# Optimization experiments

Hardware: AMD Instinct MI355X
Metric: run time of the kernel (lower is better)

The kernel has to match this reference:

```python
import jax, jax.numpy as jnp
import numpy as np

N = 16383        # complete binary tree, 14 levels
D_NODE = 512
D_SSM = 512
D_STATE = 16
MAX_DEPTH = 14   # number of BFS levels (depth 0..13)
LN_EPS = 1e-5


def setup_inputs() -> dict:
    key = jax.random.key(0)
    ks = jax.random.split(key, 8)
    # tree structure: parent[i] = (i-1)//2, root has parent -1; BFS order == index order
    parent = np.concatenate([np.array([-1]), (np.arange(1, N) - 1) // 2]).astype(np.int64)
    depth = np.floor(np.log2(np.arange(N) + 1)).astype(np.int32)
    s = jax.random.normal(ks[0], (N, D_NODE), jnp.float32)
    w = jax.random.uniform(ks[1], (N,), jnp.float32, minval=0.01, maxval=1.0)
    # parameters (xavier-ish scales)
    W_in = jax.random.normal(ks[2], (D_SSM, D_NODE + 1), jnp.float32) * (1.0 / np.sqrt(D_NODE + 1))
    b_in = jnp.zeros((D_SSM,), jnp.float32)
    W_delta = jax.random.normal(ks[3], (D_SSM, D_SSM), jnp.float32) * (1.0 / np.sqrt(D_SSM))
    # dt-style bias init: softplus(b) ~ dt in [1e-3, 1e-1]
    dt = jnp.exp(jax.random.uniform(ks[4], (D_SSM,), jnp.float32) * (np.log(0.1) - np.log(0.001)) + np.log(0.001))
    b_delta = dt + jnp.log(-jnp.expm1(-dt))
    W_w = jax.random.normal(ks[5], (D_SSM, 1), jnp.float32)
    b_w = jnp.zeros((D_SSM,), jnp.float32)
    A_log = jnp.log(jnp.broadcast_to(jnp.arange(1.0, D_STATE + 1.0, dtype=jnp.float32)[None, :], (D_SSM, D_STATE)))
    D = jnp.ones((D_SSM,), jnp.float32)
    W_B = jax.random.normal(ks[6], (D_STATE, D_SSM), jnp.float32) * (1.0 / np.sqrt(D_SSM))
    b_B = jnp.zeros((D_STATE,), jnp.float32)
    W_C = jax.random.normal(ks[7], (D_STATE, D_SSM), jnp.float32) * (1.0 / np.sqrt(D_SSM))
    b_C = jnp.zeros((D_STATE,), jnp.float32)
    gamma = jnp.ones((D_SSM,), jnp.float32)
    beta = jnp.zeros((D_SSM,), jnp.float32)
    return {"s": s, "w": w, "parent": jnp.asarray(parent), "depth": jnp.asarray(depth),
            "W_in": W_in, "b_in": b_in, "W_delta": W_delta, "b_delta": b_delta,
            "W_w": W_w, "b_w": b_w, "A_log": A_log, "D": D,
            "W_B": W_B, "b_B": b_B, "W_C": W_C, "b_C": b_C,
            "gamma": gamma, "beta": beta}


def reference(s, w, parent, depth, W_in, b_in, W_delta, b_delta, W_w, b_w,
              A_log, D, W_B, b_B, W_C, b_C, gamma, beta):
    n = s.shape[0]
    log_w = jnp.log(w + 1e-6)[:, None]                       # [N, 1]
    feat = jnp.concatenate([s, log_w], axis=1)               # [N, d_node+1]
    x = feat @ W_in.T + b_in                                 # [N, d_ssm]
    delta = jax.nn.softplus(x @ W_delta.T + b_delta) * jax.nn.sigmoid(log_w @ W_w.T + b_w)  # [N, d_ssm]
    A = -jnp.exp(A_log)                                      # [d_ssm, d_state]
    B = x @ W_B.T + b_B                                      # [N, d_state]
    C = x @ W_C.T + b_C                                      # [N, d_state]
    A_bar = jnp.exp(delta[:, :, None] * A[None])             # [N, d_ssm, d_state]
    Bx = (delta * x)[:, :, None] * B[:, None, :]             # [N, d_ssm, d_state]
    # level-parallel tree scan: all nodes at BFS depth l updated together
    par = jnp.maximum(parent, 0)
    has_par = (parent >= 0)[:, None, None]
    H = jnp.zeros((n, A_bar.shape[1], A_bar.shape[2]), x.dtype)
    for lvl in range(MAX_DEPTH):
        h_par = jnp.where(has_par, jnp.take(H, par, axis=0), 0.0)
        H = jnp.where((depth == lvl)[:, None, None], A_bar * h_par + Bx, H)
    Y = jnp.einsum('nds,ns->nd', H, C) + D * x               # [N, d_ssm]
    mu = jnp.mean(Y, axis=-1, keepdims=True)
    var = jnp.var(Y, axis=-1, keepdims=True)
    return (Y - mu) / jnp.sqrt(var + LN_EPS) * gamma + beta
```

## Files before the change

kernel.cpp:

```cpp
#include <hip/hip_runtime.h>
#include <hip/hip_bf16.h>
#include <math.h>

#define D_SSM 512
#define D_STATE 16
#define CKPT_BASE 511
#define N_CKPT 512
#define MPAD 16384

typedef __attribute__((ext_vector_type(8))) short short8;
typedef __attribute__((ext_vector_type(4))) float floatx4;

__device__ __forceinline__ unsigned short f2bf(float f) {
    unsigned int u = __float_as_uint(f);
    unsigned int r = (u + 0x7fffu + ((u >> 16) & 1u)) >> 16;
    return (unsigned short)r;
}
__device__ __forceinline__ float bf2f(unsigned short u) {
    return __uint_as_float(((unsigned int)u) << 16);
}
__device__ __forceinline__ void g2lds16(const void* g, void* l) {
    __builtin_amdgcn_global_load_lds(
        (const __attribute__((address_space(1))) void*)g,
        (__attribute__((address_space(3))) void*)l, 16, 0, 0);
}

__device__ __forceinline__ void pw_powers(float r, float* p) {
    float r2 = r * r, r4 = r2 * r2, r8 = r4 * r4;
    p[0] = r;          p[1] = r2;         p[2] = r2 * r;     p[3] = r4;
    p[4] = r4 * r;     p[5] = r4 * r2;    p[6] = r4 * p[2];  p[7] = r8;
    p[8] = r8 * r;     p[9] = r8 * r2;    p[10] = r8 * p[2]; p[11] = r8 * r4;
    p[12] = r8 * p[4]; p[13] = r8 * p[5]; p[14] = r8 * p[6]; p[15] = r8 * r8;
}

__global__ __launch_bounds__(256) void prep_kernel(
    const float* __restrict__ s, const float* __restrict__ w,
    const float* __restrict__ W_in, const float* __restrict__ W_delta,
    const float* __restrict__ W_B, const float* __restrict__ W_C,
    const float* __restrict__ A_log,
    unsigned short* __restrict__ s_bf, float* __restrict__ lw,
    unsigned short* __restrict__ Win_bf, unsigned short* __restrict__ Wd_bf,
    float* __restrict__ As_tab, int* __restrict__ fast_tab,
    int Nn)
{
    const int b = blockIdx.x, t = threadIdx.x;
    if (b < 2048) {
        #pragma unroll
        for (int rr = 0; rr < 8; rr++) {
            int row = b * 8 + rr;
            unsigned int pack = 0;
            if (row < Nn) {
                float2 sv = *(const float2*)(s + (size_t)row * 512 + t * 2);
                pack = (unsigned int)f2bf(sv.x) | ((unsigned int)f2bf(sv.y) << 16);
            }
            *(unsigned int*)(s_bf + (size_t)row * 512 + t * 2) = pack;
            if (t == 0) lw[row] = (row < Nn) ? logf(w[row] + 1e-6f) : 0.f;
        }
    } else if (b < 2048 + 512) {
        int c = b - 2048;
        float a0 = W_in[(size_t)c * 513 + t * 2];
        float a1 = W_in[(size_t)c * 513 + t * 2 + 1];
        *(unsigned int*)(Win_bf + (size_t)c * 512 + t * 2) =
            (unsigned int)f2bf(a0) | ((unsigned int)f2bf(a1) << 16);
    } else if (b < 2048 + 1024) {
        int c = b - 2048 - 512;
        float2 wv = *(const float2*)(W_delta + (size_t)c * 512 + t * 2);
        *(unsigned int*)(Wd_bf + (size_t)c * 512 + t * 2) =
            (unsigned int)f2bf(wv.x) | ((unsigned int)f2bf(wv.y) << 16);
    } else if (b < 2048 + 1024 + 128) {
        int c = b - 2048 - 1024;
        float2 wv; wv.x = 0.f; wv.y = 0.f;
        if (c < 16)      wv = *(const float2*)(W_B + (size_t)c * 512 + t * 2);
        else if (c < 32) wv = *(const float2*)(W_C + (size_t)(c - 16) * 512 + t * 2);
        *(unsigned int*)(Wd_bf + (size_t)(512 + c) * 512 + t * 2) =
            (unsigned int)f2bf(wv.x) | ((unsigned int)f2bf(wv.y) << 16);
    } else {
        int ch = (b - (2048 + 1024 + 128)) * 256 + t;
        float As0 = -__expf(A_log[ch * 16]);
        bool ok = true;
        #pragma unroll
        for (int q = 1; q < 16; q++) {
            float As = -__expf(A_log[ch * 16 + q]);
            ok = ok && (fabsf(As - (float)(q + 1) * As0) <= 1e-4f * (float)(q + 1));
        }
        As_tab[ch] = As0;
        fast_tab[ch] = ok ? 1 : 0;
    }
}

__global__ __launch_bounds__(256) void gemm_mfma(
    const unsigned short* __restrict__ Abf,
    const unsigned short* __restrict__ Wbf,
    float* __restrict__ outf,
    unsigned short* __restrict__ outbf,
    const float* __restrict__ bias,
    const float* __restrict__ lw,
    const float* __restrict__ wcol, int wcol_stride,
    const float* __restrict__ bw,
    const float* __restrict__ b_B, const float* __restrict__ b_C,
    float* __restrict__ Bm, float* __restrict__ Cm,
    int mode)
{
    __shared__ __align__(16) short As[2][128 * 32];
    __shared__ __align__(16) short Bs[2][128 * 32];
    const int tid = threadIdx.x;
    const int wave = tid >> 6, lane = tid & 63;

    const int nwg  = gridDim.x * gridDim.y;
    const int orig = blockIdx.y * gridDim.x + blockIdx.x;
    const int wsw  = (orig & 7) * (nwg >> 3) + (orig >> 3);
    const int bx   = wsw % gridDim.x;
    const int by   = wsw / gridDim.x;
    const int row0 = by * 128;
    const int col0 = bx * 128;

    const int wr = (wave >> 1) * 64;
    const int wc = (wave & 1) * 64;

    floatx4 acc[4][4] = {};

    const int srow = lane >> 2;
    const int sg   = (lane & 3) ^ ((srow >> 1) & 3);
    const int scol = sg * 8;

    const unsigned short* Ag = Abf + (size_t)(row0 + wave * 16 + srow) * 512 + scol;
    const unsigned short* Wg = Wbf + (size_t)(col0 + wave * 16 + srow) * 512 + scol;
    char* Al = (char*)&As[0][0] + wave * 1024;
    char* Bl = (char*)&Bs[0][0] + wave * 1024;

    #define STAGE(buf, k0)                                              \
        do {                                                            \
            g2lds16(Ag + (k0),            Al + (buf) * 8192);           \
            g2lds16(Ag + 64 * 512 + (k0), Al + (buf) * 8192 + 4096);    \
            g2lds16(Wg + (k0),            Bl + (buf) * 8192);           \
            g2lds16(Wg + 64 * 512 + (k0), Bl + (buf) * 8192 + 4096);    \
        } while (0)

    STAGE(0, 0);
    __syncthreads();

    for (int it = 0; it < 16; ++it) {
        const int cur = it & 1;
        if (it < 15) STAGE(cur ^ 1, (it + 1) * 32);

        short8 af[4], bfr[4];
        #pragma unroll
        for (int i = 0; i < 4; i++) {
            int m = wr + i * 16 + (lane & 15);
            int gm = (lane >> 4) ^ ((m >> 1) & 3);
            af[i] = *(const short8*)&As[cur][m * 32 + gm * 8];
        }
        #pragma unroll
        for (int j = 0; j < 4; j++) {
            int n = wc + j * 16 + (lane & 15);
            int gn = (lane >> 4) ^ ((n >> 1) & 3);
            bfr[j] = *(const short8*)&Bs[cur][n * 32 + gn * 8];
        }
        #pragma unroll
        for (int i = 0; i < 4; i++)
            #pragma unroll
            for (int j = 0; j < 4; j++)
                acc[i][j] = __builtin_amdgcn_mfma_f32_16x16x32_bf16(af[i], bfr[j], acc[i][j], 0, 0, 0);
        __syncthreads();
    }
    #undef STAGE

    if (col0 >= 512) {
        #pragma unroll
        for (int i = 0; i < 4; i++) {
            #pragma unroll
            for (int reg = 0; reg < 4; reg++) {
                int r = row0 + wr + i * 16 + (lane >> 4) * 4 + reg;
                #pragma unroll
                for (int j = 0; j < 4; j++) {
                    int c2 = wc + j * 16 + (lane & 15);
                    float z = acc[i][j][reg];
                    if (c2 < 16)      Bm[(size_t)r * 16 + c2]        = z + b_B[c2];
                    else if (c2 < 32) Cm[(size_t)r * 16 + (c2 - 16)] = z + b_C[c2 - 16];
                }
            }
        }
        return;
    }

    #pragma unroll
    for (int i = 0; i < 4; i++) {
        #pragma unroll
        for (int reg = 0; reg < 4; reg++) {
            int r = row0 + wr + i * 16 + (lane >> 4) * 4 + reg;
            float lwr = lw[r];
            #pragma unroll
            for (int j = 0; j < 4; j++) {
                int c = col0 + wc + j * 16 + (lane & 15);
                float z = acc[i][j][reg] + bias[c];
                if (mode == 0) {
                    float o = z + lwr * wcol[(size_t)c * wcol_stride];
                    outbf[(size_t)r * 512 + c] = f2bf(o);
                } else {
                    float sp = (z > 15.f) ? z : __logf(1.f + __expf(z));
                    float sg2 = __builtin_amdgcn_rcpf(1.f + __expf(-(lwr * wcol[c] + bw[c])));
                    outf[(size_t)r * 512 + c] = sp * sg2;
                }
            }
        }
    }
}

__global__ __launch_bounds__(512) void scan_fused(
    const unsigned short* __restrict__ x_bf, const float* __restrict__ delta,
    const float* __restrict__ Bm, const float* __restrict__ Cm,
    const float* __restrict__ A_log, const float* __restrict__ Dv,
    const float* __restrict__ gamma, const float* __restrict__ beta,
    const float* __restrict__ As_tab, const int* __restrict__ fast_tab,
    float* __restrict__ out)
{
    __shared__ __align__(16) float SMEM[16 * 512 + 31 * 32 + 10 * 16];
    __shared__ int nid[16];
    const int bid = blockIdx.x;
    const int d = threadIdx.x;

    const float As0 = As_tab[d];
    const bool fast = fast_tab[d] != 0;
    const float dvd = Dv[d];

    if (bid < 2 * N_CKPT) {
        const int p  = bid & 511;
        const int c0 = bid >> 9;
        const int a9 = CKPT_BASE + p;
        float* const Yb   = SMEM;
        float* const BCs  = SMEM + 8192;
        float* const Banc = SMEM + 8192 + 992;

        for (int idx = d; idx < 31 * 32; idx += 512) {
            int i = idx >> 5, c = idx & 31;
            int v = i + 1;
            int j = 31 - __builtin_clz((unsigned)v);
            int node = ((a9 + 1) << j) - 1 + (v - (1 << j));
            BCs[i * 32 + c] = (c < 16) ? Bm[(size_t)node * 16 + c]
                                       : Cm[(size_t)node * 16 + (c - 16)];
        }
        if (d < 160) {
            int k = d >> 4, ss = d & 15;
            int a = a9;
            for (int q = 0; q < k; q++) a = (a - 1) >> 1;
            Banc[k * 16 + ss] = Bm[(size_t)a * 16 + ss];
        }

        const int n10 = 2 * a9 + 1 + c0;
        float cd, nd1, nd2, nd3;
        unsigned short cx, nx1, nx2, nx3;
        cd  = delta[(size_t)n10 * 512 + d];
        cx  = x_bf[(size_t)n10 * 512 + d];
        nd1 = delta[(size_t)(2 * n10 + 1) * 512 + d];
        nx1 = x_bf[(size_t)(2 * n10 + 1) * 512 + d];
        nd2 = delta[(size_t)(4 * n10 + 3) * 512 + d];
        nx2 = x_bf[(size_t)(4 * n10 + 3) * 512 + d];

        int aB = (a9 - 1) >> 1;
        float adA = delta[(size_t)a9 * 512 + d];
        float adB = delta[(size_t)aB * 512 + d];
        unsigned short axA = x_bf[(size_t)a9 * 512 + d];
        unsigned short axB = x_bf[(size_t)aB * 512 + d];
        int anext = (aB - 1) >> 1;

        __syncthreads();

        float H9v[16];
        #pragma unroll
        for (int ss = 0; ss < 16; ss++) H9v[ss] = 0.f;
        float xv0 = 0.f;
        {
            float cum = 0.f;
            #pragma unroll
            for (int k = 0; k < 10; k++) {
                float da = adA;
                float xvk = bf2f(axA);
                if (k == 0) xv0 = xvk;
                adA = adB; axA = axB;
                if (k < 8) {
                    adB = delta[(size_t)anext * 512 + d];
                    axB = x_bf[(size_t)anext * 512 + d];
                    anext = (anext - 1) >> 1;
                }
                float bx = da * xvk;
                if (fast) {
                    float r = __expf(As0 * cum);
                    float pw[16]; pw_powers(r, pw);
                    const floatx4* B4 = (const floatx4*)&Banc[k * 16];
                    #pragma unroll
                    for (int q = 0; q < 4; q++) {
                        floatx4 b = B4[q];
                        #pragma unroll
                        for (int u = 0; u < 4; u++) {
                            int ss = q * 4 + u;
                            H9v[ss] = fmaf(bx * pw[ss], b[u], H9v[ss]);
                        }
                    }
                } else {
                    #pragma unroll
                    for (int ss = 0; ss < 16; ss++) {
                        float As = -__expf(A_log[d * 16 + ss]);
                        H9v[ss] = fmaf(bx * __expf(As * cum), Banc[k * 16 + ss], H9v[ss]);
                    }
                }
                cum += da;
            }
        }

        auto stepf = [&](int n, int bfs, float dlt, unsigned short xraw,
                         const float* Hp, float* Hc, int slot) {
            float xv = bf2f(xraw);
            float bx = dlt * xv;
            const floatx4* B4 = (const floatx4*)&BCs[bfs * 32];
            const floatx4* C4 = (const floatx4*)&BCs[bfs * 32 + 16];
            float y0 = 0.f, y1 = 0.f;
            if (fast) {
                float r = __expf(As0 * dlt);
                float pw[16]; pw_powers(r, pw);
                #pragma unroll
                for (int q = 0; q < 4; q++) {
                    floatx4 b = B4[q], c = C4[q];
                    #pragma unroll
                    for (int u = 0; u < 4; u++) {
                        int ss = q * 4 + u;
                        Hc[ss] = fmaf(pw[ss], Hp[ss], bx * b[u]);
                        if (ss & 1) y1 = fmaf(c[u], Hc[ss], y1);
                        else        y0 = fmaf(c[u], Hc[ss], y0);
                    }
                }
            } else {
                #pragma unroll
                for (int ss = 0; ss < 16; ss++) {
                    float Ab = __expf(dlt * (-__expf(A_log[d * 16 + ss])));
                    Hc[ss] = fmaf(Ab, Hp[ss], bx * BCs[bfs * 32 + ss]);
                    float cc = BCs[bfs * 32 + 16 + ss];
                    if (ss & 1) y1 = fmaf(cc, Hc[ss], y1);
                    else        y0 = fmaf(cc, Hc[ss], y0);
                }
            }
            Yb[slot * 512 + d] = fmaf(dvd, xv, y0 + y1);
            if (d == 0) nid[slot] = n;
        };
        auto leaff = [&](int n, int bfs, float dlt, unsigned short xraw,
                         const float* Hp, int slot) {
            float xv = bf2f(xraw);
            float bx = dlt * xv;
            const floatx4* B4 = (const floatx4*)&BCs[bfs * 32];
            const floatx4* C4 = (const floatx4*)&BCs[bfs * 32 + 16];
            float y0 = 0.f, y1 = 0.f;
            if (fast) {
                float r = __expf(As0 * dlt);
                float pw[16]; pw_powers(r, pw);
                #pragma unroll
                for (int q = 0; q < 4; q++) {
                    floatx4 b = B4[q], c = C4[q];
                    #pragma unroll
                    for (int u = 0; u < 4; u++) {
                        int ss = q * 4 + u;
                        float h = fmaf(pw[ss], Hp[ss], bx * b[u]);
                        if (ss & 1) y1 = fmaf(c[u], h, y1);
                        else        y0 = fmaf(c[u], h, y0);
                    }
                }
            } else {
                #pragma unroll
                for (int ss = 0; ss < 16; ss++) {
                    float Ab = __expf(dlt * (-__expf(A_log[d * 16 + ss])));
                    float h = fmaf(Ab, Hp[ss], bx * BCs[bfs * 32 + ss]);
                    float cc = BCs[bfs * 32 + 16 + ss];
                    if (ss & 1) y1 = fmaf(cc, h, y1);
                    else        y0 = fmaf(cc, h, y0);
                }
            }
            Yb[slot * 512 + d] = fmaf(dvd, xv, y0 + y1);
            if (d == 0) nid[slot] = n;
        };

        int slot = 0;
        if (c0 == 0) {
            const floatx4* C4 = (const floatx4*)&BCs[16];
            float y0 = 0.f, y1 = 0.f;
            #pragma unroll
            for (int q = 0; q < 4; q++) {
                floatx4 c = C4[q];
                #pragma unroll
                for (int u = 0; u < 4; u++) {
                    int ss = q * 4 + u;
                    if (ss & 1) y1 = fmaf(c[u], H9v[ss], y1);
                    else        y0 = fmaf(c[u], H9v[ss], y0);
                }
            }
            Yb[d] = fmaf(dvd, xv0, y0 + y1);
            if (d == 0) nid[0] = a9;
            slot = 1;
        }

        float H10[16], H11[16], H12[16];
        #define PREF(NODE) do { nd3 = delta[(size_t)(NODE) * 512 + d]; \
                                nx3 = x_bf[(size_t)(NODE) * 512 + d]; } while (0)
        #define ROT() do { cd = nd1; cx = nx1; nd1 = nd2; nx1 = nx2; \
                           nd2 = nd3; nx2 = nx3; } while (0)
        PREF(8 * n10 + 7);   stepf(n10,          1 + c0,    cd, cx, H9v, H10, slot++); ROT();
        PREF(8 * n10 + 8);   stepf(2 * n10 + 1,  3 + 2*c0,  cd, cx, H10, H11, slot++); ROT();
        PREF(4 * n10 + 4);   stepf(4 * n10 + 3,  7 + 4*c0,  cd, cx, H11, H12, slot++); ROT();
        PREF(8 * n10 + 9);   leaff(8 * n10 + 7,  15 + 8*c0, cd, cx, H12, slot++); ROT();
        PREF(8 * n10 + 10);  leaff(8 * n10 + 8,  16 + 8*c0, cd, cx, H12, slot++); ROT();
        PREF(2 * n10 + 2);   stepf(4 * n10 + 4,  8 + 4*c0,  cd, cx, H11, H12, slot++); ROT();
        PREF(4 * n10 + 5);   leaff(8 * n10 + 9,  17 + 8*c0, cd, cx, H12, slot++); ROT();
        PREF(8 * n10 + 11);  leaff(8 * n10 + 10, 18 + 8*c0, cd, cx, H12, slot++); ROT();
        PREF(8 * n10 + 12);  stepf(2 * n10 + 2,  4 + 2*c0,  cd, cx, H10, H11, slot++); ROT();
        PREF(4 * n10 + 6);   stepf(4 * n10 + 5,  9 + 4*c0,  cd, cx, H11, H12, slot++); ROT();
        PREF(8 * n10 + 13);  leaff(8 * n10 + 11, 19 + 8*c0, cd, cx, H12, slot++); ROT();
        PREF(8 * n10 + 14);  leaff(8 * n10 + 12, 20 + 8*c0, cd, cx, H12, slot++); ROT();
                             stepf(4 * n10 + 6,  10 + 4*c0, cd, cx, H11, H12, slot++); ROT();
                             leaff(8 * n10 + 13, 21 + 8*c0, cd, cx, H12, slot++); ROT();
                             leaff(8 * n10 + 14, 22 + 8*c0, cd, cx, H12, slot++);
        #undef PREF
        #undef ROT
        __syncthreads();

        const int cnt = (c0 == 0) ? 16 : 15;
        const int w = d >> 6, lane = d & 63;
        for (int i = w; i < cnt; i += 8) {
            int n = nid[i];
            float v[8]; float s1 = 0.f, s2 = 0.f;
            #pragma unroll
            for (int k = 0; k < 8; k++) {
                v[k] = Yb[i * 512 + lane + 64 * k];
                s1 += v[k]; s2 += v[k] * v[k];
            }
            #pragma unroll
            for (int off = 32; off > 0; off >>= 1) {
                s1 += __shfl_xor(s1, off);
                s2 += __shfl_xor(s2, off);
            }
            float mu = s1 * (1.f / 512.f);
            float inv = rsqrtf(s2 * (1.f / 512.f) - mu * mu + 1e-5f);
            #pragma unroll
            for (int k = 0; k < 8; k++) {
                int ch = lane + 64 * k;
                out[(size_t)n * 512 + ch] = (v[k] - mu) * inv * gamma[ch] + beta[ch];
            }
        }
    } else {
        const int n = bid - 2 * N_CKPT;
        float* const Banc9 = SMEM;
        float* const Cn    = SMEM + 144;
        float* const red   = SMEM + 160;

        if (d < 144) {
            int k = d >> 4, ss = d & 15;
            int a = n;
            for (int q = 0; q < 9; q++) if (q < k) a = (a < 0) ? -1 : ((a - 1) >> 1);
            Banc9[k * 16 + ss] = (a >= 0) ? Bm[(size_t)a * 16 + ss] : 0.f;
        }
        if (d >= 240 && d < 256) Cn[d - 240] = Cm[(size_t)n * 16 + (d - 240)];

        float adl[9]; unsigned short axr[9];
        {
            int a = n;
            #pragma unroll
            for (int k = 0; k < 9; k++) {
                bool v = a >= 0;
                adl[k] = v ? delta[(size_t)a * 512 + d] : 0.f;
                axr[k] = v ? x_bf[(size_t)a * 512 + d] : (unsigned short)0;
                a = v ? ((a - 1) >> 1) : -1;
            }
        }
        __syncthreads();

        float acc[16];
        #pragma unroll
        for (int ss = 0; ss < 16; ss++) acc[ss] = 0.f;

        float cum = 0.f;
        #pragma unroll
        for (int k = 0; k < 9; k++) {
            float da = adl[k];
            float bx = da * bf2f(axr[k]);
            if (fast) {
                float r = __expf(As0 * cum);
                float pw[16]; pw_powers(r, pw);
                const floatx4* B4 = (const floatx4*)&Banc9[k * 16];
                #pragma unroll
                for (int q = 0; q < 4; q++) {
                    floatx4 b = B4[q];
                    #pragma unroll
                    for (int u = 0; u < 4; u++) {
                        int ss = q * 4 + u;
                        acc[ss] = fmaf(bx * pw[ss], b[u], acc[ss]);
                    }
                }
            } else {
                #pragma unroll
                for (int ss = 0; ss < 16; ss++) {
                    float As = -__expf(A_log[d * 16 + ss]);
                    acc[ss] = fmaf(bx * __expf(As * cum), Banc9[k * 16 + ss], acc[ss]);
                }
            }
            cum += da;
        }

        float xv = bf2f(axr[0]);
        float y0 = 0.f, y1 = 0.f;
        const floatx4* C4 = (const floatx4*)&Cn[0];
        #pragma unroll
        for (int q = 0; q < 4; q++) {
            floatx4 c = C4[q];
            #pragma unroll
            for (int u = 0; u < 4; u++) {
                int ss = q * 4 + u;
                if (ss & 1) y1 = fmaf(c[u], acc[ss], y1);
                else        y0 = fmaf(c[u], acc[ss], y0);
            }
        }
        float y = fmaf(dvd, xv, y0 + y1);

        float s1 = y, s2 = y * y;
        #pragma unroll
        for (int off = 32; off > 0; off >>= 1) {
            s1 += __shfl_xor(s1, off);
            s2 += __shfl_xor(s2, off);
        }
        int wid = d >> 6, lane = d & 63;
        if (lane == 0) { red[wid] = s1; red[wid + 8] = s2; }
        __syncthreads();
        float S1 = 0.f, S2 = 0.f;
        #pragma unroll
        for (int k = 0; k < 8; k++) { S1 += red[k]; S2 += red[k + 8]; }
        float mu = S1 * (1.f / 512.f);
        float var = S2 * (1.f / 512.f) - mu * mu;
        float inv = rsqrtf(var + 1e-5f);
        out[(size_t)n * 512 + d] = (y - mu) * inv * gamma[d] + beta[d];
    }
}

extern "C" void kernel_launch(void* const* d_in, const int* in_sizes, int n_in,
                              void* d_out, int out_size, void* d_ws, size_t ws_size,
                              hipStream_t stream) {
    const float* s_in   = (const float*)d_in[0];
    const float* w      = (const float*)d_in[1];
    const float* W_in    = (const float*)d_in[4];
    const float* b_in    = (const float*)d_in[5];
    const float* W_delta = (const float*)d_in[6];
    const float* b_delta = (const float*)d_in[7];
    const float* W_w     = (const float*)d_in[8];
    const float* b_w     = (const float*)d_in[9];
    const float* A_log   = (const float*)d_in[10];
    const float* Dv      = (const float*)d_in[11];
    const float* W_B     = (const float*)d_in[12];
    const float* b_B     = (const float*)d_in[13];
    const float* W_C     = (const float*)d_in[14];
    const float* b_C     = (const float*)d_in[15];
    const float* gamma   = (const float*)d_in[16];
    const float* beta    = (const float*)d_in[17];
    float* out = (float*)d_out;

    const int Nn = in_sizes[1];

    float* ws    = (float*)d_ws;
    float* lw    = ws;
    float* delta = lw + MPAD;
    float* Bm    = delta + (size_t)MPAD * 512;
    float* Cm    = Bm + (size_t)MPAD * 16;
    unsigned short* s_bf  = (unsigned short*)(Cm + (size_t)MPAD * 16);
    unsigned short* x_bf  = s_bf + (size_t)MPAD * 512;
    unsigned short* Win_bf = x_bf + (size_t)MPAD * 512;
    unsigned short* Wd_bf  = Win_bf + 512 * 512;
    float* As_tab  = (float*)(Wd_bf + 640 * 512);
    int*   fast_tab = (int*)(As_tab + 512);

    prep_kernel<<<2048 + 1024 + 128 + 2, 256, 0, stream>>>(
        s_in, w, W_in, W_delta, W_B, W_C, A_log,
        s_bf, lw, Win_bf, Wd_bf, As_tab, fast_tab, Nn);

    dim3 g1(4, 128);
    gemm_mfma<<<g1, 256, 0, stream>>>(s_bf, Win_bf, nullptr, x_bf,
                                      b_in, lw, W_in + 512, 513, nullptr,
                                      nullptr, nullptr, nullptr, nullptr, 0);
    dim3 g2(5, 128);
    gemm_mfma<<<g2, 256, 0, stream>>>(x_bf, Wd_bf, delta, nullptr,
                                      b_delta, lw, W_w, 1, b_w,
                                      b_B, b_C, Bm, Cm, 1);

    scan_fused<<<2 * N_CKPT + CKPT_BASE, 512, 0, stream>>>(
        x_bf, delta, Bm, Cm, A_log, Dv, gamma, beta, As_tab, fast_tab, out);
}
```

Baseline: 215.6 us.

## Merge both checkpoint subtrees into one block to share ancestor scan work

Each checkpoint block now processes both child subtrees of its level-9 node instead of launching two blocks, one per child. Each child previously recomputed the ancestor chain state (H9) and the shared loads. The merged block computes it once, flushes layer norm output between the two subtrees, and halves the number of checkpoint blocks. The cost is less parallelism (fewer, longer blocks) and an extra barrier and flush phase inside each block.

```diff
diff --git a/kernel.cpp b/kernel.cpp
--- a/kernel.cpp
+++ b/kernel.cpp
@@ -223,10 +223,10 @@
     const bool fast = fast_tab[d] != 0;
     const float dvd = Dv[d];
 
-    if (bid < 2 * N_CKPT) {
-        const int p  = bid & 511;
-        const int c0 = bid >> 9;
-        const int a9 = CKPT_BASE + p;
+    if (bid < N_CKPT) {
+        const int a9 = CKPT_BASE + bid;
+        const int t0 = 2 * a9 + 1;
+        const int t1 = 2 * a9 + 2;
         float* const Yb   = SMEM;
         float* const BCs  = SMEM + 8192;
         float* const Banc = SMEM + 8192 + 992;
@@ -246,15 +246,12 @@
             Banc[k * 16 + ss] = Bm[(size_t)a * 16 + ss];
         }
 
-        const int n10 = 2 * a9 + 1 + c0;
-        float cd, nd1, nd2, nd3;
-        unsigned short cx, nx1, nx2, nx3;
-        cd  = delta[(size_t)n10 * 512 + d];
-        cx  = x_bf[(size_t)n10 * 512 + d];
-        nd1 = delta[(size_t)(2 * n10 + 1) * 512 + d];
-        nx1 = x_bf[(size_t)(2 * n10 + 1) * 512 + d];
-        nd2 = delta[(size_t)(4 * n10 + 3) * 512 + d];
-        nx2 = x_bf[(size_t)(4 * n10 + 3) * 512 + d];
+        float cd, nd1, nd2;
+        unsigned short cx, nx1, nx2;
+        cd  = delta[(size_t)t0 * 512 + d];
+        cx  = x_bf[(size_t)t0 * 512 + d];
+        nd1 = delta[(size_t)(2 * t0 + 1) * 512 + d];
+        nx1 = x_bf[(size_t)(2 * t0 + 1) * 512 + d];
 
         int aB = (a9 - 1) >> 1;
         float adA = delta[(size_t)a9 * 512 + d];
@@ -375,9 +372,32 @@
             Yb[slot * 512 + d] = fmaf(dvd, xv, y0 + y1);
             if (d == 0) nid[slot] = n;
         };
-
-        int slot = 0;
-        if (c0 == 0) {
+        auto flush = [&](int cnt) {
+            const int w = d >> 6, lane = d & 63;
+            for (int i = w; i < cnt; i += 8) {
+                int n = nid[i];
+                float v[8]; float s1 = 0.f, s2 = 0.f;
+                #pragma unroll
+                for (int k = 0; k < 8; k++) {
+                    v[k] = Yb[i * 512 + lane + 64 * k];
+                    s1 += v[k]; s2 += v[k] * v[k];
+                }
+                #pragma unroll
+                for (int off = 32; off > 0; off >>= 1) {
+                    s1 += __shfl_xor(s1, off);
+                    s2 += __shfl_xor(s2, off);
+                }
+                float mu = s1 * (1.f / 512.f);
+                float inv = rsqrtf(s2 * (1.f / 512.f) - mu * mu + 1e-5f);
+                #pragma unroll
+                for (int k = 0; k < 8; k++) {
+                    int ch = lane + 64 * k;
+                    out[(size_t)n * 512 + ch] = (v[k] - mu) * inv * gamma[ch] + beta[ch];
+                }
+            }
+        };
+
+        {
             const floatx4* C4 = (const floatx4*)&BCs[16];
             float y0 = 0.f, y1 = 0.f;
             #pragma unroll
@@ -392,58 +412,51 @@
             }
             Yb[d] = fmaf(dvd, xv0, y0 + y1);
             if (d == 0) nid[0] = a9;
-            slot = 1;
         }
 
         float H10[16], H11[16], H12[16];
-        #define PREF(NODE) do { nd3 = delta[(size_t)(NODE) * 512 + d]; \
-                                nx3 = x_bf[(size_t)(NODE) * 512 + d]; } while (0)
-        #define ROT() do { cd = nd1; cx = nx1; nd1 = nd2; nx1 = nx2; \
-                           nd2 = nd3; nx2 = nx3; } while (0)
-        PREF(8 * n10 + 7);   stepf(n10,          1 + c0,    cd, cx, H9v, H10, slot++); ROT();
-        PREF(8 * n10 + 8);   stepf(2 * n10 + 1,  3 + 2*c0,  cd, cx, H10, H11, slot++); ROT();
-        PREF(4 * n10 + 4);   stepf(4 * n10 + 3,  7 + 4*c0,  cd, cx, H11, H12, slot++); ROT();
-        PREF(8 * n10 + 9);   leaff(8 * n10 + 7,  15 + 8*c0, cd, cx, H12, slot++); ROT();
-        PREF(8 * n10 + 10);  leaff(8 * n10 + 8,  16 + 8*c0, cd, cx, H12, slot++); ROT();
-        PREF(2 * n10 + 2);   stepf(4 * n10 + 4,  8 + 4*c0,  cd, cx, H11, H12, slot++); ROT();
-        PREF(4 * n10 + 5);   leaff(8 * n10 + 9,  17 + 8*c0, cd, cx, H12, slot++); ROT();
-        PREF(8 * n10 + 11);  leaff(8 * n10 + 10, 18 + 8*c0, cd, cx, H12, slot++); ROT();
-        PREF(8 * n10 + 12);  stepf(2 * n10 + 2,  4 + 2*c0,  cd, cx, H10, H11, slot++); ROT();
-        PREF(4 * n10 + 6);   stepf(4 * n10 + 5,  9 + 4*c0,  cd, cx, H11, H12, slot++); ROT();
-        PREF(8 * n10 + 13);  leaff(8 * n10 + 11, 19 + 8*c0, cd, cx, H12, slot++); ROT();
-        PREF(8 * n10 + 14);  leaff(8 * n10 + 12, 20 + 8*c0, cd, cx, H12, slot++); ROT();
-                             stepf(4 * n10 + 6,  10 + 4*c0, cd, cx, H11, H12, slot++); ROT();
-                             leaff(8 * n10 + 13, 21 + 8*c0, cd, cx, H12, slot++); ROT();
-                             leaff(8 * n10 + 14, 22 + 8*c0, cd, cx, H12, slot++);
+        #define PREF(NODE) do { nd2 = delta[(size_t)(NODE) * 512 + d]; \
+                                nx2 = x_bf[(size_t)(NODE) * 512 + d]; } while (0)
+        #define ROT() do { cd = nd1; cx = nx1; nd1 = nd2; nx1 = nx2; } while (0)
+        PREF(4 * t0 + 3);   stepf(t0,          1,  cd, cx, H9v, H10, 1);  ROT();
+        PREF(8 * t0 + 7);   stepf(2 * t0 + 1,  3,  cd, cx, H10, H11, 2);  ROT();
+        PREF(8 * t0 + 8);   stepf(4 * t0 + 3,  7,  cd, cx, H11, H12, 3);  ROT();
+        PREF(4 * t0 + 4);   leaff(8 * t0 + 7,  15, cd, cx, H12, 4);  ROT();
+        PREF(8 * t0 + 9);   leaff(8 * t0 + 8,  16, cd, cx, H12, 5);  ROT();
+        PREF(8 * t0 + 10);  stepf(4 * t0 + 4,  8,  cd, cx, H11, H12, 6);  ROT();
+        PREF(2 * t0 + 2);   leaff(8 * t0 + 9,  17, cd, cx, H12, 7);  ROT();
+        PREF(4 * t0 + 5);   leaff(8 * t0 + 10, 18, cd, cx, H12, 8);  ROT();
+        PREF(8 * t0 + 11);  stepf(2 * t0 + 2,  4,  cd, cx, H10, H11, 9);  ROT();
+        PREF(8 * t0 + 12);  stepf(4 * t0 + 5,  9,  cd, cx, H11, H12, 10); ROT();
+        PREF(4 * t0 + 6);   leaff(8 * t0 + 11, 19, cd, cx, H12, 11); ROT();
+        PREF(8 * t0 + 13);  leaff(8 * t0 + 12, 20, cd, cx, H12, 12); ROT();
+        PREF(8 * t0 + 14);  stepf(4 * t0 + 6,  10, cd, cx, H11, H12, 13); ROT();
+        PREF(t1);           leaff(8 * t0 + 13, 21, cd, cx, H12, 14); ROT();
+        PREF(2 * t1 + 1);   leaff(8 * t0 + 14, 22, cd, cx, H12, 15); ROT();
+        __syncthreads();
+        flush(16);
+        __syncthreads();
+        PREF(4 * t1 + 3);   stepf(t1,          2,  cd, cx, H9v, H10, 0);  ROT();
+        PREF(8 * t1 + 7);   stepf(2 * t1 + 1,  5,  cd, cx, H10, H11, 1);  ROT();
+        PREF(8 * t1 + 8);   stepf(4 * t1 + 3,  11, cd, cx, H11, H12, 2);  ROT();
+        PREF(4 * t1 + 4);   leaff(8 * t1 + 7,  23, cd, cx, H12, 3);  ROT();
+        PREF(8 * t1 + 9);   leaff(8 * t1 + 8,  24, cd, cx, H12, 4);  ROT();
+        PREF(8 * t1 + 10);  stepf(4 * t1 + 4,  12, cd, cx, H11, H12, 5);  ROT();
+        PREF(2 * t1 + 2);   leaff(8 * t1 + 9,  25, cd, cx, H12, 6);  ROT();
+        PREF(4 * t1 + 5);   leaff(8 * t1 + 10, 26, cd, cx, H12, 7);  ROT();
+        PREF(8 * t1 + 11);  stepf(2 * t1 + 2,  6,  cd, cx, H10, H11, 8);  ROT();
+        PREF(8 * t1 + 12);  stepf(4 * t1 + 5,  13, cd, cx, H11, H12, 9);  ROT();
+        PREF(4 * t1 + 6);   leaff(8 * t1 + 11, 27, cd, cx, H12, 10); ROT();
+        PREF(8 * t1 + 13);  leaff(8 * t1 + 12, 28, cd, cx, H12, 11); ROT();
+        PREF(8 * t1 + 14);  stepf(4 * t1 + 6,  14, cd, cx, H11, H12, 12); ROT();
+                            leaff(8 * t1 + 13, 29, cd, cx, H12, 13); ROT();
+                            leaff(8 * t1 + 14, 30, cd, cx, H12, 14);
         #undef PREF
         #undef ROT
         __syncthreads();
-
-        const int cnt = (c0 == 0) ? 16 : 15;
-        const int w = d >> 6, lane = d & 63;
-        for (int i = w; i < cnt; i += 8) {
-            int n = nid[i];
-            float v[8]; float s1 = 0.f, s2 = 0.f;
-            #pragma unroll
-            for (int k = 0; k < 8; k++) {
-                v[k] = Yb[i * 512 + lane + 64 * k];
-                s1 += v[k]; s2 += v[k] * v[k];
-            }
-            #pragma unroll
-            for (int off = 32; off > 0; off >>= 1) {
-                s1 += __shfl_xor(s1, off);
-                s2 += __shfl_xor(s2, off);
-            }
-            float mu = s1 * (1.f / 512.f);
-            float inv = rsqrtf(s2 * (1.f / 512.f) - mu * mu + 1e-5f);
-            #pragma unroll
-            for (int k = 0; k < 8; k++) {
-                int ch = lane + 64 * k;
-                out[(size_t)n * 512 + ch] = (v[k] - mu) * inv * gamma[ch] + beta[ch];
-            }
-        }
+        flush(15);
     } else {
-        const int n = bid - 2 * N_CKPT;
+        const int n = bid - N_CKPT;
         float* const Banc9 = SMEM;
         float* const Cn    = SMEM + 144;
         float* const red   = SMEM + 160;
@@ -583,6 +596,6 @@
                                       b_delta, lw, W_w, 1, b_w,
                                       b_B, b_C, Bm, Cm, 1);
 
-    scan_fused<<<2 * N_CKPT + CKPT_BASE, 512, 0, stream>>>(
+    scan_fused<<<N_CKPT + CKPT_BASE, 512, 0, stream>>>(
         x_bf, delta, Bm, Cm, A_log, Dv, gamma, beta, As_tab, fast_tab, out);
 }
```

Measured after the change: 248.1 us. 15.1% more time.
